# Kernel optimization log

Measured on AMD Instinct MI355X. Metric: run time of the kernel, lower is better.

The kernel has to match this reference:

```python
import jax, jax.numpy as jnp
import numpy as np

B, TQ, TKV, D, H = 4, 1024, 2048, 1024, 16
DH = D // H


def setup_inputs() -> dict:
    key = jax.random.key(0)
    ks = jax.random.split(key, 12)
    s = 0.02
    return {
        "x": jax.random.normal(ks[0], (B, TQ, D), jnp.float32),
        "k_cache": jax.random.normal(ks[1], (B, TKV, D), jnp.float32),
        "v_cache": jax.random.normal(ks[2], (B, TKV, D), jnp.float32),
        "mask": jnp.zeros((TQ, TKV), jnp.float32),  # additive attention bias
        "Wq": jax.random.normal(ks[3], (D, D), jnp.float32) * s,
        "bq": jax.random.normal(ks[4], (D,), jnp.float32) * s,
        "Wk": jax.random.normal(ks[5], (D, D), jnp.float32) * s,  # key: no bias (Whisper-style)
        "Wv": jax.random.normal(ks[6], (D, D), jnp.float32) * s,
        "bv": jax.random.normal(ks[7], (D,), jnp.float32) * s,
        "Wo": jax.random.normal(ks[8], (D, D), jnp.float32) * s,
        "bo": jax.random.normal(ks[9], (D,), jnp.float32) * s,
    }


def reference(x, k_cache, v_cache, mask, Wq, bq, Wk, Wv, bv, Wo, bo):
    b, tq, d = x.shape
    scale = (d // H) ** -0.25
    # QKV projections (torch Linear: y = x @ W.T + b)
    q = x @ Wq.T + bq                      # [B,Tq,D]
    k_new = x @ Wk.T                       # [B,Tq,D] (key has no bias)
    v_new = x @ Wv.T + bv                  # [B,Tq,D]
    # KV-cache append: write last Tq positions
    k_cache = k_cache.at[:, -tq:, :].set(k_new)
    v_cache = v_cache.at[:, -tq:, :].set(v_new)
    # split heads
    qh = q.reshape(b, tq, H, DH) * scale           # [B,Tq,H,Dh]
    kh = k_cache.reshape(b, -1, H, DH) * scale     # [B,Tkv,H,Dh]
    vh = v_cache.reshape(b, -1, H, DH)             # [B,Tkv,H,Dh]
    qk = jnp.einsum("bqhd,bkhd->bhqk", qh, kh) + mask  # [B,H,Tq,Tkv]
    w = jax.nn.softmax(qk.astype(jnp.float32), axis=-1).astype(qh.dtype)
    wv = jnp.einsum("bhqk,bkhd->bqhd", w, vh).reshape(b, tq, d)
    out = wv @ Wo.T + bo
    return out, k_cache, v_cache
```

## Files before the change

kernel.cpp:

```cpp
#include <hip/hip_runtime.h>
#include <hip/hip_bf16.h>


typedef __bf16 bf16_t;
typedef __attribute__((ext_vector_type(4))) float f32x4;
typedef __attribute__((ext_vector_type(8))) __bf16 bf16x8;
typedef __attribute__((ext_vector_type(4))) __bf16 bf16x4;

__device__ inline bf16x4 cvt4(float4 f) {
    bf16x4 o;
    o.x = (bf16_t)f.x; o.y = (bf16_t)f.y; o.z = (bf16_t)f.z; o.w = (bf16_t)f.w;
    return o;
}

__device__ inline void gload_lds16(const void* g, void* s) {
    __builtin_amdgcn_global_load_lds(
        (const __attribute__((address_space(1))) void*)g,
        (__attribute__((address_space(3))) void*)s, 16, 0, 0);
}


__global__ void cast_f32_bf16_k(const float* __restrict__ src, bf16_t* __restrict__ dst, int n4) {
    int i = blockIdx.x * blockDim.x + threadIdx.x;
    if (i >= n4) return;
    float4 f = reinterpret_cast<const float4*>(src)[i];
    reinterpret_cast<bf16x4*>(dst)[i] = cvt4(f);
}

__global__ void build_wqkv_k(const float* __restrict__ Wq, const float* __restrict__ Wk,
                             const float* __restrict__ Wv, bf16_t* __restrict__ dst) {
    int i = blockIdx.x * blockDim.x + threadIdx.x;
    if (i >= 786432) return;
    int e0 = i * 4;
    int row = e0 >> 10;
    const float* src;
    if (row < 1024)       src = Wq + e0;
    else if (row < 2048)  src = Wk + (e0 - 1048576);
    else                  src = Wv + (e0 - 2097152);
    float4 f = *reinterpret_cast<const float4*>(src);
    reinterpret_cast<bf16x4*>(dst)[i] = cvt4(f);
}

__global__ void build_bias_k(const float* __restrict__ bq, const float* __restrict__ bv,
                             float* __restrict__ bias) {
    int i = blockIdx.x * blockDim.x + threadIdx.x;
    if (i >= 3072) return;
    float v;
    if (i < 1024)      v = bq[i];
    else if (i < 2048) v = 0.f;
    else               v = bv[i - 2048];
    bias[i] = v;
}

__global__ void copy_old2_k(const float* __restrict__ kc, const float* __restrict__ vc,
                            float* __restrict__ kout, float* __restrict__ vout,
                            bf16_t* __restrict__ k_bf) {
    int i = blockIdx.x * blockDim.x + threadIdx.x;
    if (i >= 2097152) return;
    int which = i >> 20;
    int ii = i & 1048575;
    int b = ii >> 18;
    int r = ii & 262143;
    size_t off = (size_t)b * 2097152 + (size_t)r * 4;
    if (which == 0) {
        float4 f = *reinterpret_cast<const float4*>(kc + off);
        *reinterpret_cast<float4*>(kout + off) = f;
        reinterpret_cast<bf16x4*>(k_bf + off)[0] = cvt4(f);
    } else {
        float4 f = *reinterpret_cast<const float4*>(vc + off);
        *reinterpret_cast<float4*>(vout + off) = f;
    }
}

__global__ __launch_bounds__(256) void transpose_v_k(const float* __restrict__ vout,
                                                     bf16_t* __restrict__ vT) {
    __shared__ bf16_t t[64][65];
    int blk = blockIdx.x;
    int kvt = blk >> 6;
    int bh  = blk & 63;
    int b = bh >> 4, h = bh & 15;
    int kv0 = kvt * 64;
    int tid = threadIdx.x;
    int c = tid & 63, r0 = tid >> 6;
    #pragma unroll
    for (int rr = r0; rr < 64; rr += 4)
        t[rr][c] = (bf16_t)vout[((size_t)b * 2048 + kv0 + rr) * 1024 + h * 64 + c];
    __syncthreads();
    #pragma unroll
    for (int dd = r0; dd < 64; dd += 4)
        vT[((size_t)bh * 64 + dd) * 2048 + kv0 + c] = t[c][dd];
}

__global__ void mask_frag_k(const float* __restrict__ mask, float* __restrict__ maskF) {
    int i = blockIdx.x * blockDim.x + threadIdx.x;
    if (i >= 2097152) return;
    int qrow = i >> 11, rem = i & 2047;
    int kvt = rem >> 6, win = rem & 63;
    int c16 = win >> 2, nt = win & 3;
    maskF[i] = mask[(size_t)qrow * 2048 + kvt * 64 + nt * 16 + c16];
}

template <int MODE>
__global__ __launch_bounds__(256) void gemm_lds_k(const bf16_t* __restrict__ A,
                                                  const bf16_t* __restrict__ Bw,
                                                  const float* __restrict__ bias,
                                                  bf16_t* __restrict__ q_bf,
                                                  float* __restrict__ kout,
                                                  bf16_t* __restrict__ k_bf,
                                                  float* __restrict__ vout,
                                                  float* __restrict__ out0) {
    const int K = 1024;
    __shared__ __align__(16) bf16_t As[2][4096];
    __shared__ __align__(16) bf16_t Bs[2][4096];
    int m0 = blockIdx.x * 128, n0 = blockIdx.y * 128;
    int tid = threadIdx.x;
    int lane = tid & 63, w = tid >> 6;
    int wr = w >> 1, wc = w & 1;
    int col16 = lane & 15, quad = lane >> 4;
    int mbase = m0 + wr * 64, nbase = n0 + wc * 64;

    int srow = tid >> 2;
    int scol = (tid & 3) * 8;
    const bf16_t* ga = A + (size_t)(m0 + srow) * K + scol;
    const bf16_t* gb = Bw + (size_t)(n0 + srow) * K + scol;

    f32x4 zero = {0.f, 0.f, 0.f, 0.f};
    f32x4 acc[4][4];
    #pragma unroll
    for (int mi = 0; mi < 4; mi++)
        #pragma unroll
        for (int ni = 0; ni < 4; ni++) acc[mi][ni] = zero;

    auto stageg = [&](int d, int k) {
        gload_lds16(ga + k, &As[d][tid * 8]);
        gload_lds16(ga + (size_t)64 * K + k, &As[d][tid * 8 + 2048]);
        gload_lds16(gb + k, &Bs[d][tid * 8]);
        gload_lds16(gb + (size_t)64 * K + k, &Bs[d][tid * 8 + 2048]);
    };

    stageg(0, 0);
    __syncthreads();
    for (int kb = 0; kb < 32; kb++) {
        int cur = kb & 1;
        if (kb < 31) stageg(cur ^ 1, (kb + 1) * 32);
        bf16x8 af[4], bfr[4];
        #pragma unroll
        for (int mi = 0; mi < 4; mi++)
            af[mi] = *reinterpret_cast<const bf16x8*>(
                &As[cur][(wr * 64 + mi * 16 + col16) * 32 + quad * 8]);
        #pragma unroll
        for (int ni = 0; ni < 4; ni++)
            bfr[ni] = *reinterpret_cast<const bf16x8*>(
                &Bs[cur][(wc * 64 + ni * 16 + col16) * 32 + quad * 8]);
        #pragma unroll
        for (int mi = 0; mi < 4; mi++)
            #pragma unroll
            for (int ni = 0; ni < 4; ni++)
                acc[mi][ni] = __builtin_amdgcn_mfma_f32_16x16x32_bf16(
                    af[mi], bfr[ni], acc[mi][ni], 0, 0, 0);
        __syncthreads();
    }

    #pragma unroll
    for (int mi = 0; mi < 4; mi++) {
        #pragma unroll
        for (int ni = 0; ni < 4; ni++) {
            int gm_base = mbase + mi * 16 + quad * 4;
            int gn = nbase + ni * 16 + col16;
            float bia = bias[gn];
            #pragma unroll
            for (int r = 0; r < 4; r++) {
                int gm = gm_base + r;
                float v = acc[mi][ni][r] + bia;
                if (MODE == 0) {
                    if (gn < 1024) {
                        q_bf[(size_t)gm * 1024 + gn] = (bf16_t)v;
                    } else if (gn < 2048) {
                        int n2 = gn - 1024;
                        int b = gm >> 10, t = gm & 1023;
                        size_t off = ((size_t)b * 2048 + 1024 + t) * 1024 + n2;
                        kout[off] = v;
                        k_bf[off] = (bf16_t)v;
                    } else {
                        int n2 = gn - 2048;
                        int b = gm >> 10, t = gm & 1023;
                        vout[((size_t)b * 2048 + 1024 + t) * 1024 + n2] = v;
                    }
                } else {
                    out0[(size_t)gm * 1024 + gn] = v;
                }
            }
        }
    }
}

__global__ __launch_bounds__(128) void attn_k(const bf16_t* __restrict__ qbf,
                                              const bf16_t* __restrict__ kbf,
                                              const bf16_t* __restrict__ vT,
                                              const float* __restrict__ maskF,
                                              bf16_t* __restrict__ wv) {
    __shared__ __align__(16) bf16_t Ks[2][4096];
    __shared__ __align__(16) bf16_t Vs[2][4096];
    __shared__ __align__(16) bf16_t plds[2][32 * 64];
    int blk = blockIdx.x;
    int qt = blk >> 6;
    int bh = blk & 63;
    int b = bh >> 4, h = bh & 15;
    int tid = threadIdx.x, w = tid >> 6, lane = tid & 63;
    int col16 = lane & 15, quad = lane >> 4;
    int c7 = col16 & 7, c3 = col16 >> 3;
    int qr0 = qt * 64 + w * 32;

    const bf16_t* kg[4]; const bf16_t* vg[4]; int sl[4];
    #pragma unroll
    for (int j = 0; j < 4; j++) {
        int s = tid + 128 * j;
        int r = s >> 3, c = (s & 7) ^ (r & 7);
        kg[j] = kbf + ((size_t)b * 2048 + r) * 1024 + h * 64 + c * 8;
        vg[j] = vT + ((size_t)bh * 64 + r) * 2048 + c * 8;
        sl[j] = s * 8;
    }
    auto stage = [&](int d, int kv0) {
        #pragma unroll
        for (int j = 0; j < 4; j++) {
            gload_lds16(kg[j] + (size_t)kv0 * 1024, &Ks[d][sl[j]]);
            gload_lds16(vg[j] + kv0, &Vs[d][sl[j]]);
        }
    };

    const bf16_t* qrow = qbf + ((size_t)b * 1024 + qr0 + col16) * 1024 + h * 64;
    bf16x8 aq[2][2];
    #pragma unroll
    for (int mi = 0; mi < 2; mi++) {
        aq[mi][0] = *reinterpret_cast<const bf16x8*>(qrow + mi * 16384 + quad * 8);
        aq[mi][1] = *reinterpret_cast<const bf16x8*>(qrow + mi * 16384 + 32 + quad * 8);
    }

    const float* mbase = maskF + (size_t)(qr0 + quad * 4) * 2048 + col16 * 4;
    int cx = (quad ^ c7) * 8;

    f32x4 zero = {0.f, 0.f, 0.f, 0.f};
    float lrow[2][4];
    f32x4 oacc[2][4];
    #pragma unroll
    for (int mi = 0; mi < 2; mi++)
        #pragma unroll
        for (int r = 0; r < 4; r++) { lrow[mi][r] = 0.f; oacc[mi][r] = zero; }

    stage(0, 0);
    __syncthreads();

    for (int t = 0; t < 32; t++) {
        int cur = t & 1;
        int kv0 = t * 64;
        if (t < 31) stage(cur ^ 1, kv0 + 64);
        f32x4 mf[2][4];
        #pragma unroll
        for (int mi = 0; mi < 2; mi++)
            #pragma unroll
            for (int r = 0; r < 4; r++)
                mf[mi][r] = *reinterpret_cast<const f32x4*>(
                    mbase + (size_t)(mi * 16 + r) * 2048 + kv0);
        f32x4 s[2][4];
        #pragma unroll
        for (int nt = 0; nt < 4; nt++) {
            const bf16_t* kr = &Ks[cur][(nt * 16 + col16) * 64];
            bf16x8 k0 = *reinterpret_cast<const bf16x8*>(kr + cx);
            bf16x8 k1 = *reinterpret_cast<const bf16x8*>(kr + (cx ^ 32));
            #pragma unroll
            for (int mi = 0; mi < 2; mi++) {
                s[mi][nt] = __builtin_amdgcn_mfma_f32_16x16x32_bf16(aq[mi][0], k0, zero, 0, 0, 0);
                s[mi][nt] = __builtin_amdgcn_mfma_f32_16x16x32_bf16(aq[mi][1], k1, s[mi][nt], 0, 0, 0);
            }
        }
        #pragma unroll
        for (int mi = 0; mi < 2; mi++)
            #pragma unroll
            for (int r = 0; r < 4; r++) {
                int rb = quad * 4 + r;
                int rowoff = (mi * 16 + rb) * 64 + c7;
                #pragma unroll
                for (int nt = 0; nt < 4; nt++) {
                    float p = __expf(s[mi][nt][r] * 0.125f + mf[mi][r][nt]);
                    lrow[mi][r] += p;
                    int sw = (nt * 2 + c3) ^ (rb & 7);
                    plds[w][rowoff + sw * 8] = (bf16_t)p;
                }
            }
        bf16x8 pf[2][2];
        #pragma unroll
        for (int mi = 0; mi < 2; mi++)
            #pragma unroll
            for (int half = 0; half < 2; half++)
                pf[mi][half] = *reinterpret_cast<const bf16x8*>(
                    &plds[w][(mi * 16 + col16) * 64 + (((half * 4 + quad) ^ c7) * 8)]);
        #pragma unroll
        for (int dt = 0; dt < 4; dt++) {
            const bf16_t* vr = &Vs[cur][(dt * 16 + col16) * 64];
            bf16x8 v0 = *reinterpret_cast<const bf16x8*>(vr + cx);
            bf16x8 v1 = *reinterpret_cast<const bf16x8*>(vr + (cx ^ 32));
            #pragma unroll
            for (int mi = 0; mi < 2; mi++) {
                oacc[mi][dt] = __builtin_amdgcn_mfma_f32_16x16x32_bf16(pf[mi][0], v0, oacc[mi][dt], 0, 0, 0);
                oacc[mi][dt] = __builtin_amdgcn_mfma_f32_16x16x32_bf16(pf[mi][1], v1, oacc[mi][dt], 0, 0, 0);
            }
        }
        __syncthreads();
    }

    #pragma unroll
    for (int d = 1; d < 16; d <<= 1)
        #pragma unroll
        for (int mi = 0; mi < 2; mi++)
            #pragma unroll
            for (int r = 0; r < 4; r++) lrow[mi][r] += __shfl_xor(lrow[mi][r], d);
    #pragma unroll
    for (int mi = 0; mi < 2; mi++) {
        float inv[4];
        #pragma unroll
        for (int r = 0; r < 4; r++) inv[r] = 1.f / lrow[mi][r];
        #pragma unroll
        for (int dt = 0; dt < 4; dt++)
            #pragma unroll
            for (int r = 0; r < 4; r++)
                wv[((size_t)b * 1024 + qr0 + mi * 16 + quad * 4 + r) * 1024 +
                   h * 64 + dt * 16 + col16] = (bf16_t)(oacc[mi][dt][r] * inv[r]);
    }
}


extern "C" void kernel_launch(void* const* d_in, const int* in_sizes, int n_in,
                              void* d_out, int out_size, void* d_ws, size_t ws_size,
                              hipStream_t stream) {
    const float* x    = (const float*)d_in[0];
    const float* kc   = (const float*)d_in[1];
    const float* vc   = (const float*)d_in[2];
    const float* mask = (const float*)d_in[3];
    const float* Wq   = (const float*)d_in[4];
    const float* bq   = (const float*)d_in[5];
    const float* Wk   = (const float*)d_in[6];
    const float* Wv   = (const float*)d_in[7];
    const float* bv   = (const float*)d_in[8];
    const float* Wo   = (const float*)d_in[9];
    const float* bo   = (const float*)d_in[10];

    float* out0 = (float*)d_out;
    float* kout = out0 + 4194304;
    float* vout = out0 + 12582912;

    char* ws = (char*)d_ws;
    bf16_t* x_bf     = (bf16_t*)(ws);
    bf16_t* wqkv_bf  = (bf16_t*)(ws + 8388608);
    bf16_t* wo_bf    = (bf16_t*)(ws + 14680064);
    float*  bias_qkv = (float*)(ws + 16777216);
    bf16_t* q_bf     = (bf16_t*)(ws + 16789504);
    bf16_t* k_bf     = (bf16_t*)(ws + 25178112);
    bf16_t* vT_bf    = (bf16_t*)(ws + 41955328);
    bf16_t* wv_bf    = (bf16_t*)(ws + 58732544);
    float*  maskF    = (float*)(ws + 67108864);

    cast_f32_bf16_k<<<4096, 256, 0, stream>>>(x, x_bf, 1048576);
    build_wqkv_k<<<3072, 256, 0, stream>>>(Wq, Wk, Wv, wqkv_bf);
    cast_f32_bf16_k<<<1024, 256, 0, stream>>>(Wo, wo_bf, 262144);
    build_bias_k<<<12, 256, 0, stream>>>(bq, bv, bias_qkv);
    mask_frag_k<<<8192, 256, 0, stream>>>(mask, maskF);
    copy_old2_k<<<8192, 256, 0, stream>>>(kc, vc, kout, vout, k_bf);
    gemm_lds_k<0><<<dim3(32, 24), 256, 0, stream>>>(x_bf, wqkv_bf, bias_qkv,
                                                    q_bf, kout, k_bf, vout, nullptr);
    transpose_v_k<<<2048, 256, 0, stream>>>(vout, vT_bf);
    attn_k<<<1024, 128, 0, stream>>>(q_bf, k_bf, vT_bf, maskF, wv_bf);
    gemm_lds_k<1><<<dim3(32, 8), 256, 0, stream>>>(wv_bf, wo_bf, bo,
                                                   nullptr, nullptr, nullptr, nullptr, out0);
}
```

Measured before the change: 333.8 us.

## Keep softmax probabilities in registers via permlane swaps and bf16 mask

The attention kernel is restructured. Each block now has 8 waves of 16 query rows, and the MFMA operands are swapped so that S^T is computed. The probability tile is repacked into the PV operand with v_cvt_pk_bf16 and permlane32/16 swaps, which removes the LDS round trip through plds. The mask is pre-scaled by log2(e), stored as bf16 in a fragment-friendly order, and applied with exp2. Block ids are remapped so that blocks sharing K/V land near each other. This halves mask traffic and removes LDS stores and loads, at the cost of bf16 precision on the mask and per-wave MFMA work that covers only 16 rows.

```diff
diff --git a/kernel.cpp b/kernel.cpp
--- a/kernel.cpp
+++ b/kernel.cpp
@@ -6,6 +6,7 @@
 typedef __attribute__((ext_vector_type(4))) float f32x4;
 typedef __attribute__((ext_vector_type(8))) __bf16 bf16x8;
 typedef __attribute__((ext_vector_type(4))) __bf16 bf16x4;
+typedef __attribute__((ext_vector_type(4))) unsigned short u16x4;
 
 __device__ inline bf16x4 cvt4(float4 f) {
     bf16x4 o;
@@ -18,6 +19,24 @@
         (const __attribute__((address_space(1))) void*)g,
         (__attribute__((address_space(3))) void*)s, 16, 0, 0);
 }
+
+__device__ inline unsigned cvt_pk_bf16(float lo, float hi) {
+    unsigned r;
+    asm("v_cvt_pk_bf16_f32 %0, %1, %2" : "=v"(r) : "v"(lo), "v"(hi));
+    return r;
+}
+__device__ inline void pswap32(unsigned& a, unsigned& b) {
+    asm("v_permlane32_swap_b32 %0, %1" : "+v"(a), "+v"(b));
+}
+__device__ inline void pswap16(unsigned& a, unsigned& b) {
+    asm("v_permlane16_swap_b32 %0, %1" : "+v"(a), "+v"(b));
+}
+
+#if __has_builtin(__builtin_amdgcn_exp2f)
+__device__ inline float exp2_fast(float x) { return __builtin_amdgcn_exp2f(x); }
+#else
+__device__ inline float exp2_fast(float x) { return exp2f(x); }
+#endif
 
 
 __global__ void cast_f32_bf16_k(const float* __restrict__ src, bf16_t* __restrict__ dst, int n4) {
@@ -91,13 +110,16 @@
         vT[((size_t)bh * 64 + dd) * 2048 + kv0 + c] = t[c][dd];
 }
 
-__global__ void mask_frag_k(const float* __restrict__ mask, float* __restrict__ maskF) {
+__global__ void mask_bf16_k(const float* __restrict__ mask, bf16_t* __restrict__ maskB) {
     int i = blockIdx.x * blockDim.x + threadIdx.x;
     if (i >= 2097152) return;
-    int qrow = i >> 11, rem = i & 2047;
-    int kvt = rem >> 6, win = rem & 63;
-    int c16 = win >> 2, nt = win & 3;
-    maskF[i] = mask[(size_t)qrow * 2048 + kvt * 64 + nt * 16 + c16];
+    int r   = i & 3;
+    int c16 = (i >> 2) & 15;
+    int qd  = (i >> 6) & 3;
+    int kb  = (i >> 8) & 127;
+    int qb  = i >> 15;
+    float v = mask[(size_t)(qb * 16 + c16) * 2048 + kb * 16 + qd * 4 + r] * 1.4426950408889634f;
+    maskB[i] = (bf16_t)v;
 }
 
 template <int MODE>
@@ -194,137 +216,105 @@
     }
 }
 
-__global__ __launch_bounds__(128) void attn_k(const bf16_t* __restrict__ qbf,
-                                              const bf16_t* __restrict__ kbf,
-                                              const bf16_t* __restrict__ vT,
-                                              const float* __restrict__ maskF,
-                                              bf16_t* __restrict__ wv) {
+__global__ __launch_bounds__(512, 4) void attn_k(const bf16_t* __restrict__ qbf,
+                                                 const bf16_t* __restrict__ kbf,
+                                                 const bf16_t* __restrict__ vT,
+                                                 const bf16_t* __restrict__ maskB,
+                                                 bf16_t* __restrict__ wv) {
     __shared__ __align__(16) bf16_t Ks[2][4096];
     __shared__ __align__(16) bf16_t Vs[2][4096];
-    __shared__ __align__(16) bf16_t plds[2][32 * 64];
-    int blk = blockIdx.x;
-    int qt = blk >> 6;
-    int bh = blk & 63;
+    int logical = (blockIdx.x & 7) * 64 + (blockIdx.x >> 3);
+    int bh = logical >> 3;
+    int qtb = logical & 7;
     int b = bh >> 4, h = bh & 15;
     int tid = threadIdx.x, w = tid >> 6, lane = tid & 63;
     int col16 = lane & 15, quad = lane >> 4;
-    int c7 = col16 & 7, c3 = col16 >> 3;
-    int qr0 = qt * 64 + w * 32;
-
-    const bf16_t* kg[4]; const bf16_t* vg[4]; int sl[4];
-    #pragma unroll
-    for (int j = 0; j < 4; j++) {
-        int s = tid + 128 * j;
-        int r = s >> 3, c = (s & 7) ^ (r & 7);
-        kg[j] = kbf + ((size_t)b * 2048 + r) * 1024 + h * 64 + c * 8;
-        vg[j] = vT + ((size_t)bh * 64 + r) * 2048 + c * 8;
-        sl[j] = s * 8;
-    }
+    int c7 = col16 & 7;
+    int cx = (quad ^ c7) * 8;
+    int qr0 = qtb * 128 + w * 16;
+
+    int sr = tid >> 3, sc = (tid & 7) ^ ((tid >> 3) & 7);
+    const bf16_t* kg = kbf + ((size_t)b * 2048 + sr) * 1024 + h * 64 + sc * 8;
+    const bf16_t* vg = vT + ((size_t)bh * 64 + sr) * 2048 + sc * 8;
     auto stage = [&](int d, int kv0) {
-        #pragma unroll
-        for (int j = 0; j < 4; j++) {
-            gload_lds16(kg[j] + (size_t)kv0 * 1024, &Ks[d][sl[j]]);
-            gload_lds16(vg[j] + kv0, &Vs[d][sl[j]]);
-        }
+        gload_lds16(kg + (size_t)kv0 * 1024, &Ks[d][tid * 8]);
+        gload_lds16(vg + kv0, &Vs[d][tid * 8]);
     };
 
     const bf16_t* qrow = qbf + ((size_t)b * 1024 + qr0 + col16) * 1024 + h * 64;
-    bf16x8 aq[2][2];
-    #pragma unroll
-    for (int mi = 0; mi < 2; mi++) {
-        aq[mi][0] = *reinterpret_cast<const bf16x8*>(qrow + mi * 16384 + quad * 8);
-        aq[mi][1] = *reinterpret_cast<const bf16x8*>(qrow + mi * 16384 + 32 + quad * 8);
-    }
-
-    const float* mbase = maskF + (size_t)(qr0 + quad * 4) * 2048 + col16 * 4;
-    int cx = (quad ^ c7) * 8;
+    bf16x8 aq0 = *reinterpret_cast<const bf16x8*>(qrow + quad * 8);
+    bf16x8 aq1 = *reinterpret_cast<const bf16x8*>(qrow + 32 + quad * 8);
+
+    const bf16_t* mbase = maskB + (size_t)(qtb * 8 + w) * 32768 + quad * 64 + col16 * 4;
 
     f32x4 zero = {0.f, 0.f, 0.f, 0.f};
-    float lrow[2][4];
-    f32x4 oacc[2][4];
-    #pragma unroll
-    for (int mi = 0; mi < 2; mi++)
-        #pragma unroll
-        for (int r = 0; r < 4; r++) { lrow[mi][r] = 0.f; oacc[mi][r] = zero; }
+    f32x4 oacc[4];
+    #pragma unroll
+    for (int dt = 0; dt < 4; dt++) oacc[dt] = zero;
+    float lrow = 0.f;
 
     stage(0, 0);
     __syncthreads();
 
     for (int t = 0; t < 32; t++) {
         int cur = t & 1;
-        int kv0 = t * 64;
-        if (t < 31) stage(cur ^ 1, kv0 + 64);
-        f32x4 mf[2][4];
-        #pragma unroll
-        for (int mi = 0; mi < 2; mi++)
-            #pragma unroll
-            for (int r = 0; r < 4; r++)
-                mf[mi][r] = *reinterpret_cast<const f32x4*>(
-                    mbase + (size_t)(mi * 16 + r) * 2048 + kv0);
-        f32x4 s[2][4];
+        if (t < 31) stage(cur ^ 1, (t + 1) * 64);
+        unsigned pk[4][2];
         #pragma unroll
         for (int nt = 0; nt < 4; nt++) {
             const bf16_t* kr = &Ks[cur][(nt * 16 + col16) * 64];
             bf16x8 k0 = *reinterpret_cast<const bf16x8*>(kr + cx);
             bf16x8 k1 = *reinterpret_cast<const bf16x8*>(kr + (cx ^ 32));
-            #pragma unroll
-            for (int mi = 0; mi < 2; mi++) {
-                s[mi][nt] = __builtin_amdgcn_mfma_f32_16x16x32_bf16(aq[mi][0], k0, zero, 0, 0, 0);
-                s[mi][nt] = __builtin_amdgcn_mfma_f32_16x16x32_bf16(aq[mi][1], k1, s[mi][nt], 0, 0, 0);
-            }
-        }
-        #pragma unroll
-        for (int mi = 0; mi < 2; mi++)
+            f32x4 s = __builtin_amdgcn_mfma_f32_16x16x32_bf16(k0, aq0, zero, 0, 0, 0);
+            s = __builtin_amdgcn_mfma_f32_16x16x32_bf16(k1, aq1, s, 0, 0, 0);
+            u16x4 m4 = *reinterpret_cast<const u16x4*>(mbase + (size_t)(t * 4 + nt) * 256);
+            float p[4];
             #pragma unroll
             for (int r = 0; r < 4; r++) {
-                int rb = quad * 4 + r;
-                int rowoff = (mi * 16 + rb) * 64 + c7;
-                #pragma unroll
-                for (int nt = 0; nt < 4; nt++) {
-                    float p = __expf(s[mi][nt][r] * 0.125f + mf[mi][r][nt]);
-                    lrow[mi][r] += p;
-                    int sw = (nt * 2 + c3) ^ (rb & 7);
-                    plds[w][rowoff + sw * 8] = (bf16_t)p;
-                }
+                float mv = __builtin_bit_cast(float, (unsigned)m4[r] << 16);
+                p[r] = exp2_fast(fmaf(s[r], 0.18033688011112042f, mv));
+                lrow += p[r];
             }
-        bf16x8 pf[2][2];
-        #pragma unroll
-        for (int mi = 0; mi < 2; mi++)
-            #pragma unroll
-            for (int half = 0; half < 2; half++)
-                pf[mi][half] = *reinterpret_cast<const bf16x8*>(
-                    &plds[w][(mi * 16 + col16) * 64 + (((half * 4 + quad) ^ c7) * 8)]);
+            pk[nt][0] = cvt_pk_bf16(p[0], p[1]);
+            pk[nt][1] = cvt_pk_bf16(p[2], p[3]);
+        }
+        union PB { unsigned u[4]; bf16x8 v; };
+        PB pf0, pf1;
+        {
+            unsigned a0 = pk[0][0], b0 = pk[1][0];
+            pswap32(a0, b0); pswap16(a0, b0);
+            pf0.u[0] = a0; pf0.u[2] = b0;
+            unsigned a1 = pk[0][1], b1 = pk[1][1];
+            pswap32(a1, b1); pswap16(a1, b1);
+            pf0.u[1] = a1; pf0.u[3] = b1;
+            unsigned a2 = pk[2][0], b2 = pk[3][0];
+            pswap32(a2, b2); pswap16(a2, b2);
+            pf1.u[0] = a2; pf1.u[2] = b2;
+            unsigned a3 = pk[2][1], b3 = pk[3][1];
+            pswap32(a3, b3); pswap16(a3, b3);
+            pf1.u[1] = a3; pf1.u[3] = b3;
+        }
         #pragma unroll
         for (int dt = 0; dt < 4; dt++) {
             const bf16_t* vr = &Vs[cur][(dt * 16 + col16) * 64];
             bf16x8 v0 = *reinterpret_cast<const bf16x8*>(vr + cx);
             bf16x8 v1 = *reinterpret_cast<const bf16x8*>(vr + (cx ^ 32));
-            #pragma unroll
-            for (int mi = 0; mi < 2; mi++) {
-                oacc[mi][dt] = __builtin_amdgcn_mfma_f32_16x16x32_bf16(pf[mi][0], v0, oacc[mi][dt], 0, 0, 0);
-                oacc[mi][dt] = __builtin_amdgcn_mfma_f32_16x16x32_bf16(pf[mi][1], v1, oacc[mi][dt], 0, 0, 0);
-            }
+            oacc[dt] = __builtin_amdgcn_mfma_f32_16x16x32_bf16(v0, pf0.v, oacc[dt], 0, 0, 0);
+            oacc[dt] = __builtin_amdgcn_mfma_f32_16x16x32_bf16(v1, pf1.v, oacc[dt], 0, 0, 0);
         }
         __syncthreads();
     }
 
-    #pragma unroll
-    for (int d = 1; d < 16; d <<= 1)
-        #pragma unroll
-        for (int mi = 0; mi < 2; mi++)
-            #pragma unroll
-            for (int r = 0; r < 4; r++) lrow[mi][r] += __shfl_xor(lrow[mi][r], d);
-    #pragma unroll
-    for (int mi = 0; mi < 2; mi++) {
-        float inv[4];
-        #pragma unroll
-        for (int r = 0; r < 4; r++) inv[r] = 1.f / lrow[mi][r];
-        #pragma unroll
-        for (int dt = 0; dt < 4; dt++)
-            #pragma unroll
-            for (int r = 0; r < 4; r++)
-                wv[((size_t)b * 1024 + qr0 + mi * 16 + quad * 4 + r) * 1024 +
-                   h * 64 + dt * 16 + col16] = (bf16_t)(oacc[mi][dt][r] * inv[r]);
+    lrow += __shfl_xor(lrow, 16);
+    lrow += __shfl_xor(lrow, 32);
+    float inv = 1.f / lrow;
+    bf16_t* orow = wv + ((size_t)b * 1024 + qr0 + col16) * 1024 + h * 64 + quad * 4;
+    #pragma unroll
+    for (int dt = 0; dt < 4; dt++) {
+        bf16x4 o4;
+        #pragma unroll
+        for (int r = 0; r < 4; r++) o4[r] = (bf16_t)(oacc[dt][r] * inv);
+        *reinterpret_cast<bf16x4*>(orow + dt * 16) = o4;
     }
 }
 
@@ -357,18 +347,18 @@
     bf16_t* k_bf     = (bf16_t*)(ws + 25178112);
     bf16_t* vT_bf    = (bf16_t*)(ws + 41955328);
     bf16_t* wv_bf    = (bf16_t*)(ws + 58732544);
-    float*  maskF    = (float*)(ws + 67108864);
+    bf16_t* maskB    = (bf16_t*)(ws + 67108864);
 
     cast_f32_bf16_k<<<4096, 256, 0, stream>>>(x, x_bf, 1048576);
     build_wqkv_k<<<3072, 256, 0, stream>>>(Wq, Wk, Wv, wqkv_bf);
     cast_f32_bf16_k<<<1024, 256, 0, stream>>>(Wo, wo_bf, 262144);
     build_bias_k<<<12, 256, 0, stream>>>(bq, bv, bias_qkv);
-    mask_frag_k<<<8192, 256, 0, stream>>>(mask, maskF);
+    mask_bf16_k<<<8192, 256, 0, stream>>>(mask, maskB);
     copy_old2_k<<<8192, 256, 0, stream>>>(kc, vc, kout, vout, k_bf);
     gemm_lds_k<0><<<dim3(32, 24), 256, 0, stream>>>(x_bf, wqkv_bf, bias_qkv,
                                                     q_bf, kout, k_bf, vout, nullptr);
     transpose_v_k<<<2048, 256, 0, stream>>>(vout, vT_bf);
-    attn_k<<<1024, 128, 0, stream>>>(q_bf, k_bf, vT_bf, maskF, wv_bf);
+    attn_k<<<512, 512, 0, stream>>>(q_bf, k_bf, vT_bf, maskB, wv_bf);
     gemm_lds_k<1><<<dim3(32, 8), 256, 0, stream>>>(wv_bf, wo_bf, bo,
                                                    nullptr, nullptr, nullptr, nullptr, out0);
 }
```

Measured after the change: 313.5 us. 1.06x faster.
